# Kernel tuning notes

Measured on AMD Instinct MI355X. Metric: run time of the kernel, lower is better.

The kernel has to match this reference:

```python
import jax, jax.numpy as jnp
import numpy as np

B, D, S = 4, 512, 2048
H, DK = 8, 64  # d_model = H * DK
SCALE = float(np.sqrt(DK))
EPS = 1e-8


def setup_inputs() -> dict:
    key = jax.random.key(0)
    ks = jax.random.split(key, 9)
    std = (2.0 / D) ** 0.5  # kaiming_normal fan_out for 1x1 conv
    inp = {"x": jax.random.normal(ks[0], (B, D, 2, S), dtype=jnp.float32)}
    i = 1
    for n in ("q", "k", "v", "o"):
        inp[f"W{n}_r"] = jax.random.normal(ks[i], (D, D), dtype=jnp.float32) * std
        inp[f"W{n}_i"] = jax.random.normal(ks[i + 1], (D, D), dtype=jnp.float32) * std
        inp[f"b{n}_r"] = jnp.zeros((D,), dtype=jnp.float32)
        inp[f"b{n}_i"] = jnp.zeros((D,), dtype=jnp.float32)
        i += 2
    return inp


def _cconv(x, Wr, Wi, br, bi):
    # complex 1x1 conv: x [B, D, 2, S] -> [B, D, 2, S]
    real, imag = x[:, :, 0, :], x[:, :, 1, :]
    o_r = (jnp.einsum('od,bds->bos', Wr, real)
           - jnp.einsum('od,bds->bos', Wi, imag) + (br - bi)[None, :, None])
    o_i = (jnp.einsum('od,bds->bos', Wr, imag)
           + jnp.einsum('od,bds->bos', Wi, real) + (br + bi)[None, :, None])
    return jnp.stack([o_r, o_i], axis=2)


def reference(x, Wq_r, Wq_i, bq_r, bq_i, Wk_r, Wk_i, bk_r, bk_i,
              Wv_r, Wv_i, bv_r, bv_i, Wo_r, Wo_i, bo_r, bo_i):
    b, c, _, s = x.shape
    Q = _cconv(x, Wq_r, Wq_i, bq_r, bq_i).reshape(b, H, DK, 2, s)
    K = _cconv(x, Wk_r, Wk_i, bk_r, bk_i).reshape(b, H, DK, 2, s)
    V = _cconv(x, Wv_r, Wv_i, bv_r, bv_i).reshape(b, H, DK, 2, s)
    Qm = jnp.sqrt(Q[:, :, :, 0] ** 2 + Q[:, :, :, 1] ** 2 + EPS)  # [b,H,DK,s]
    Km = jnp.sqrt(K[:, :, :, 0] ** 2 + K[:, :, :, 1] ** 2 + EPS)
    scores = jnp.einsum('bhds,bhdt->bhst', Qm, Km) / SCALE  # [b,H,s,s]
    attn = jax.nn.softmax(scores, axis=-1)  # dropout is identity in eval
    Vr = jnp.einsum('bhst,bhdt->bhds', attn, V[:, :, :, 0])  # [b,H,DK,s]
    Vi = jnp.einsum('bhst,bhdt->bhds', attn, V[:, :, :, 1])
    out = jnp.stack([Vr.reshape(b, c, s), Vi.reshape(b, c, s)], axis=2)
    return _cconv(out, Wo_r, Wo_i, bo_r, bo_i)
```

## Files before the change

### kernel.cpp

```cpp
#include <hip/hip_runtime.h>
#include <math.h>
#include <stdint.h>

typedef __attribute__((ext_vector_type(8))) _Float16 f16x8;
typedef __attribute__((ext_vector_type(2))) __fp16 fp16x2;
typedef __attribute__((ext_vector_type(4))) float f32x4;
typedef __attribute__((ext_vector_type(16))) float f32x16;

static __device__ __forceinline__ unsigned short f2h(float f) {
  union { _Float16 h; unsigned short u; } v; v.h = (_Float16)f;
  return v.u;
}
static __device__ __forceinline__ float h2f(unsigned short u) {
  union { unsigned short u; _Float16 h; } v; v.u = u;
  return (float)v.h;
}
static __device__ __forceinline__ unsigned pkrtz(float a, float b) {
  union { fp16x2 h; unsigned u; } v;
  v.h = __builtin_amdgcn_cvt_pkrtz(a, b);
  return v.u;
}

#define GLOAD_LDS16(g, l) __builtin_amdgcn_global_load_lds( \
    (const __attribute__((address_space(1))) void*)(g),     \
    (__attribute__((address_space(3))) void*)(l), 16, 0, 0)

__global__ __launch_bounds__(256) void pack_w(
    const float* __restrict__ Wr, const float* __restrict__ Wi,
    const float* __restrict__ br, const float* __restrict__ bi,
    unsigned short* __restrict__ W2, float* __restrict__ bias2) {
  int idx = blockIdx.x * 256 + threadIdx.x;
  int m = idx >> 10, k = idx & 1023;
  int o = m & 511, d = k & 511;
  float v;
  if (m < 512) v = (k < 512) ? Wr[o * 512 + d] : -Wi[o * 512 + d];
  else         v = (k < 512) ? Wi[o * 512 + d] :  Wr[o * 512 + d];
  W2[idx] = f2h(v);
  if (idx < 1024) {
    int oo = idx & 511;
    bias2[idx] = (idx < 512) ? (br[oo] - bi[oo]) : (br[oo] + bi[oo]);
  }
}

__global__ __launch_bounds__(256) void pack_x(
    const float* __restrict__ x, unsigned short* __restrict__ XT) {
  __shared__ unsigned short tl[64][72];
  const int t = threadIdx.x;
  const int sBase = blockIdx.x * 64, dBase = blockIdx.y * 64;
  const int b = blockIdx.z >> 1, c = blockIdx.z & 1;
  const int r = t >> 2, cb = (t & 3) * 16;
  const float* src = x + (((size_t)(b * 512 + dBase + r) * 2 + c) * 2048 + sBase + cb);
#pragma unroll
  for (int j = 0; j < 16; j += 4) {
    float4 v = *(const float4*)(src + j);
    tl[cb + j + 0][r] = f2h(v.x);
    tl[cb + j + 1][r] = f2h(v.y);
    tl[cb + j + 2][r] = f2h(v.z);
    tl[cb + j + 3][r] = f2h(v.w);
  }
  __syncthreads();
  const int s = t >> 2, dc = (t & 3) * 16;
  unsigned short* dst = XT + ((size_t)(b * 2048 + sBase + s)) * 1024 + c * 512 + dBase + dc;
  *(uint4*)dst = *(const uint4*)&tl[s][dc];
  *(uint4*)(dst + 8) = *(const uint4*)&tl[s][dc + 8];
}

template <int MODE>
__global__ __launch_bounds__(256) void gemm_bt(
    const unsigned short* __restrict__ A, const unsigned short* __restrict__ Bt,
    const float* __restrict__ bias, unsigned short* __restrict__ Cb,
    float* __restrict__ Cf) {
  __shared__ unsigned short As[128 * 32];
  __shared__ unsigned short Bs[128 * 32];
  const int t = threadIdx.x;
  const int wave = t >> 6, lane = t & 63;
  const int wr = wave >> 1, wc = wave & 1;
  const int mBase = blockIdx.y * 128, nBase = blockIdx.x * 128;
  const int z = blockIdx.z;
  A += (size_t)z * 1024 * 1024;
  bias += z * 1024;
  if (MODE == 0) Cb += (size_t)z * 1024 * 8192;
  const int lr = lane & 15, lk = (lane >> 4) * 8;
  f32x4 acc[4][4] = {};
  const int grow = wave * 32 + (lane >> 2);
  const int gcol = (lane & 3) * 8;
  const unsigned short* ga = A + (size_t)(mBase + grow) * 1024 + gcol;
  const unsigned short* gb = Bt + (size_t)(nBase + grow) * 1024 + gcol;
  unsigned short* lA = &As[wave * 1024];
  unsigned short* lB = &Bs[wave * 1024];
  for (int k0 = 0; k0 < 1024; k0 += 32) {
    __syncthreads();
    GLOAD_LDS16(ga + k0, lA);
    GLOAD_LDS16(ga + 16 * 1024 + k0, lA + 512);
    GLOAD_LDS16(gb + k0, lB);
    GLOAD_LDS16(gb + 16 * 1024 + k0, lB + 512);
    __syncthreads();
    f16x8 af[4], bfr[4];
#pragma unroll
    for (int i = 0; i < 4; ++i) {
      af[i]  = *(const f16x8*)&As[(wr * 64 + i * 16 + lr) * 32 + lk];
      bfr[i] = *(const f16x8*)&Bs[(wc * 64 + i * 16 + lr) * 32 + lk];
    }
#pragma unroll
    for (int i = 0; i < 4; ++i)
#pragma unroll
      for (int j = 0; j < 4; ++j)
        acc[i][j] = __builtin_amdgcn_mfma_f32_16x16x32_f16(af[i], bfr[j], acc[i][j], 0, 0, 0);
  }
  const int cr = (lane >> 4) * 4, cc = lane & 15;
#pragma unroll
  for (int i = 0; i < 4; ++i) {
#pragma unroll
    for (int j = 0; j < 4; ++j) {
      const int m0 = mBase + wr * 64 + i * 16 + cr;
      const int n0 = nBase + wc * 64 + j * 16 + cc;
#pragma unroll
      for (int g = 0; g < 4; ++g) {
        float v = acc[i][j][g] + bias[m0 + g];
        if (MODE == 0) {
          const int m = m0 + g;
          if (z == 2) {
            const int ri = m >> 9, mm = m & 511;
            const int h = mm >> 6, dloc = mm & 63;
            const int jj = dloc >> 5, q31 = dloc & 31;
            const int b = n0 >> 11, s = n0 & 2047;
            const int tile = s >> 6, ks = (s >> 4) & 3, hi = (s >> 3) & 1, e = s & 7;
            const size_t flat =
                ((((((size_t)(b * 8 + h) * 32 + tile) * 4 + ks) * 2 + jj) * 2 + ri) * 64 +
                 hi * 32 + q31) * 8 + e;
            Cb[flat] = f2h(v);
          } else {
            Cb[(size_t)m * 8192 + n0] = f2h(v);
          }
        } else {
          const int m = m0 + g;
          const int c = m >> 9, o = m & 511;
          const int b = n0 >> 11, s = n0 & 2047;
          Cf[(size_t)b * 2097152 + (size_t)o * 4096 + c * 2048 + s] = v;
        }
      }
    }
  }
}

__global__ __launch_bounds__(256) void mag_qk(
    const unsigned short* __restrict__ Cq, const unsigned short* __restrict__ Ck,
    unsigned short* __restrict__ Qm, unsigned short* __restrict__ Km) {
  __shared__ unsigned short tl[64][72];
  const int isK = blockIdx.z;
  const unsigned short* C = isK ? Ck : Cq;
  unsigned short* Out = isK ? Km : Qm;
  const int t = threadIdx.x;
  const int sBase = blockIdx.x * 64;
  const int bh = blockIdx.y, b = bh >> 3, h = bh & 7;
  const int d = t >> 2, sc = (t & 3) * 16;
  const unsigned short* pr = C + (size_t)(h * 64 + d) * 8192 + b * 2048 + sBase + sc;
  const unsigned short* pi = pr + (size_t)512 * 8192;
  unsigned short rb[16], ib[16];
  *(uint4*)&rb[0] = *(const uint4*)pr;  *(uint4*)&rb[8] = *(const uint4*)(pr + 8);
  *(uint4*)&ib[0] = *(const uint4*)pi;  *(uint4*)&ib[8] = *(const uint4*)(pi + 8);
#pragma unroll
  for (int j = 0; j < 16; ++j) {
    float fr = h2f(rb[j]), fi = h2f(ib[j]);
    tl[sc + j][d] = f2h(sqrtf(fr * fr + fi * fi + 1e-8f));
  }
  __syncthreads();
  const int s = t >> 2, dc = (t & 3) * 16;
  if (isK) {
    const int kb = s >> 5, q31 = s & 31, db = dc >> 4;
    unsigned short* dstf = Out +
        ((((size_t)bh * 32 + blockIdx.x) * 2 + kb) * 4 + db) * 512 + (size_t)q31 * 8;
    *(uint4*)dstf = *(const uint4*)&tl[s][dc];
    *(uint4*)(dstf + 256) = *(const uint4*)&tl[s][dc + 8];
  } else {
    unsigned short* dst = Out + ((size_t)bh * 2048 + sBase + s) * 64 + dc;
    *(uint4*)dst = *(const uint4*)&tl[s][dc];
    *(uint4*)(dst + 8) = *(const uint4*)&tl[s][dc + 8];
  }
}

__global__ __launch_bounds__(256) void attn(
    const unsigned short* __restrict__ Qm, const unsigned short* __restrict__ Km,
    const unsigned short* __restrict__ Vf, unsigned short* __restrict__ OutT) {
  const int t = threadIdx.x, wave = t >> 6, lane = t & 63;
  const int id = blockIdx.x;
  const int xcd = id & 7, within = id >> 3;
  const int bh = xcd * 4 + (within >> 4);
  const int qtile = within & 15;
  const int b = bh >> 3, h = bh & 7;
  const int q31 = lane & 31, hi = lane >> 5;
  const int qBase = qtile * 128 + wave * 32;
  const float ls = 0.18033688f;

  f16x8 qf[4];
  {
    const unsigned short* qp = Qm + ((size_t)bh * 2048 + qBase + q31) * 64 + hi * 8;
    qf[0] = *(const f16x8*)qp;
    qf[1] = *(const f16x8*)(qp + 16);
    qf[2] = *(const f16x8*)(qp + 32);
    qf[3] = *(const f16x8*)(qp + 48);
  }
  f32x16 Or[2] = {}, Oi[2] = {};
  float m = -1e30f, l = 0.f;

  const unsigned short* kmF = Km + (size_t)bh * 131072 + (size_t)lane * 8;
  const unsigned short* vF  = Vf + (size_t)bh * 262144 + (size_t)lane * 8;

  for (int t0 = 0; t0 < 2048; t0 += 64) {
    const int tile = t0 >> 6;
    f16x8 kf[2][4];
#pragma unroll
    for (int kb = 0; kb < 2; ++kb)
#pragma unroll
      for (int db = 0; db < 4; ++db)
        kf[kb][db] = *(const f16x8*)(kmF + (size_t)(((tile * 2 + kb) * 4 + db)) * 512);
    __builtin_amdgcn_sched_barrier(0);
    f32x16 S[2] = {};
#pragma unroll
    for (int kb = 0; kb < 2; ++kb)
#pragma unroll
      for (int db = 0; db < 4; ++db)
        S[kb] = __builtin_amdgcn_mfma_f32_32x32x16_f16(kf[kb][db], qf[db], S[kb], 0, 0, 0);
    f16x8 vr[4][2], vi[4][2];
#pragma unroll
    for (int ks = 0; ks < 4; ++ks)
#pragma unroll
      for (int j = 0; j < 2; ++j) {
        const size_t u = (size_t)(((tile * 4 + ks) * 2 + j) * 2) * 512;
        vr[ks][j] = *(const f16x8*)(vF + u);
        vi[ks][j] = *(const f16x8*)(vF + u + 512);
      }
    __builtin_amdgcn_sched_barrier(0);
    float m0a = fmaxf(S[0][0], S[0][1]), m0b = fmaxf(S[0][2], S[0][3]);
#pragma unroll
    for (int r = 4; r < 16; r += 4) {
      m0a = fmaxf(m0a, fmaxf(S[0][r], S[0][r + 1]));
      m0b = fmaxf(m0b, fmaxf(S[0][r + 2], S[0][r + 3]));
    }
#pragma unroll
    for (int r = 0; r < 16; r += 4) {
      m0a = fmaxf(m0a, fmaxf(S[1][r], S[1][r + 1]));
      m0b = fmaxf(m0b, fmaxf(S[1][r + 2], S[1][r + 3]));
    }
    float vmax = fmaxf(m0a, m0b);
    vmax = fmaxf(vmax, __shfl_xor(vmax, 32, 64));
    float pmax = vmax * ls;
    if (__any(pmax > m + 8.0f)) {
      float mnew = fmaxf(m, pmax);
      float al = __builtin_amdgcn_exp2f(m - mnew);
      m = mnew;
      l *= al;
#pragma unroll
      for (int r = 0; r < 16; ++r) {
        const int qloc = (r & 3) + 8 * (r >> 2) + 4 * hi;
        float ao = __shfl(al, qloc, 64);
        Or[0][r] *= ao; Or[1][r] *= ao;
        Oi[0][r] *= ao; Oi[1][r] *= ao;
      }
    }
    float p[2][16];
    float ps0 = 0.f, ps1 = 0.f;
#pragma unroll
    for (int kb = 0; kb < 2; ++kb)
#pragma unroll
      for (int r = 0; r < 16; r += 2) {
        float pa_ = __builtin_amdgcn_exp2f(fmaf(S[kb][r], ls, -m));
        float pb_ = __builtin_amdgcn_exp2f(fmaf(S[kb][r + 1], ls, -m));
        p[kb][r] = pa_; p[kb][r + 1] = pb_;
        ps0 += pa_; ps1 += pb_;
      }
    float ps = ps0 + ps1;
    ps += __shfl_xor(ps, 32, 64);
    l += ps;
    f16x8 pa[4];
#pragma unroll
    for (int ks = 0; ks < 4; ++ks) {
      const float* pp = &p[ks >> 1][8 * (ks & 1)];
      unsigned c0 = pkrtz(pp[0], pp[1]);
      unsigned c1 = pkrtz(pp[2], pp[3]);
      unsigned d0 = pkrtz(pp[4], pp[5]);
      unsigned d1 = pkrtz(pp[6], pp[7]);
      asm volatile("v_permlane32_swap_b32 %0, %1" : "+v"(c0), "+v"(d0));
      asm volatile("v_permlane32_swap_b32 %0, %1" : "+v"(c1), "+v"(d1));
      union { unsigned u[4]; f16x8 v; } w;
      w.u[0] = c0; w.u[1] = c1; w.u[2] = d0; w.u[3] = d1;
      pa[ks] = w.v;
    }
#pragma unroll
    for (int ks = 0; ks < 4; ++ks)
#pragma unroll
      for (int j = 0; j < 2; ++j) {
        Or[j] = __builtin_amdgcn_mfma_f32_32x32x16_f16(pa[ks], vr[ks][j], Or[j], 0, 0, 0);
        Oi[j] = __builtin_amdgcn_mfma_f32_32x32x16_f16(pa[ks], vi[ks][j], Oi[j], 0, 0, 0);
      }
  }
  float linv = 1.0f / l;
#pragma unroll
  for (int r = 0; r < 16; ++r) {
    const int qloc = (r & 3) + 8 * (r >> 2) + 4 * hi;
    float iv = __shfl(linv, qloc, 64);
    unsigned short* orow = OutT + ((size_t)b * 2048 + qBase + qloc) * 1024 + h * 64;
    orow[q31]       = f2h(Or[0][r] * iv);
    orow[32 + q31]  = f2h(Or[1][r] * iv);
    orow[512 + q31] = f2h(Oi[0][r] * iv);
    orow[544 + q31] = f2h(Oi[1][r] * iv);
  }
}

extern "C" void kernel_launch(void* const* d_in, const int* in_sizes, int n_in,
                              void* d_out, int out_size, void* d_ws, size_t ws_size,
                              hipStream_t stream) {
  (void)in_sizes; (void)n_in; (void)out_size; (void)ws_size;
  const float* x = (const float*)d_in[0];

  unsigned short* XT = (unsigned short*)d_ws;
  unsigned short* W2 = XT + (size_t)8192 * 1024;
  float* bias2 = (float*)(W2 + (size_t)4 * 1024 * 1024);
  unsigned short* Cqkv = (unsigned short*)(bias2 + 4096);
  unsigned short* Qm = (unsigned short*)d_out;
  unsigned short* Km = Qm + (size_t)4 * 8 * 2048 * 64;
  unsigned short* Vf = Cqkv + (size_t)2 * 1024 * 8192;
  unsigned short* OutT = Cqkv;

  for (int s = 0; s < 4; ++s) {
    pack_w<<<4096, 256, 0, stream>>>(
        (const float*)d_in[1 + 4 * s], (const float*)d_in[2 + 4 * s],
        (const float*)d_in[3 + 4 * s], (const float*)d_in[4 + 4 * s],
        W2 + (size_t)s * 1024 * 1024, bias2 + s * 1024);
  }
  pack_x<<<dim3(32, 8, 8), 256, 0, stream>>>(x, XT);
  gemm_bt<0><<<dim3(64, 8, 3), 256, 0, stream>>>(W2, XT, bias2, Cqkv, nullptr);
  mag_qk<<<dim3(32, 32, 2), 256, 0, stream>>>(Cqkv, Cqkv + (size_t)1024 * 8192, Qm, Km);
  attn<<<512, 256, 0, stream>>>(Qm, Km, Vf, OutT);
  gemm_bt<1><<<dim3(64, 8, 1), 256, 0, stream>>>(
      W2 + (size_t)3 * 1024 * 1024, OutT, bias2 + 3 * 1024, nullptr, (float*)d_out);
}
```

Measured before the change: 209.7 us.

## Split attention over key halves with a combine kernel and XCD-aware GEMM grid

The attention kernel now splits each query tile's key range into two halves, doubling the grid to 1024 blocks for better CU occupancy. Each half writes normalized partial outputs plus its running max and sum, and a new combine kernel merges them with log-sum-exp weights. GEMM launches are flattened to 1D with an XCD-aware block remapping so neighbouring N tiles share an XCD's L2. This adds an extra kernel and extra partial-output traffic, and rounds the partial outputs to fp16 before merging.

```diff
diff --git a/kernel.cpp b/kernel.cpp
--- a/kernel.cpp
+++ b/kernel.cpp
@@ -75,8 +75,11 @@
   const int t = threadIdx.x;
   const int wave = t >> 6, lane = t & 63;
   const int wr = wave >> 1, wc = wave & 1;
-  const int mBase = blockIdx.y * 128, nBase = blockIdx.x * 128;
-  const int z = blockIdx.z;
+  const int bid = blockIdx.x;
+  const int xcd = bid & 7, g = bid >> 3;
+  const int i = g & 63, z = g >> 6;
+  const int nb = xcd * 8 + (i >> 3), mb = i & 7;
+  const int mBase = mb * 128, nBase = nb * 128;
   A += (size_t)z * 1024 * 1024;
   bias += z * 1024;
   if (MODE == 0) Cb += (size_t)z * 1024 * 8192;
@@ -97,28 +100,28 @@
     __syncthreads();
     f16x8 af[4], bfr[4];
 #pragma unroll
-    for (int i = 0; i < 4; ++i) {
-      af[i]  = *(const f16x8*)&As[(wr * 64 + i * 16 + lr) * 32 + lk];
-      bfr[i] = *(const f16x8*)&Bs[(wc * 64 + i * 16 + lr) * 32 + lk];
-    }
-#pragma unroll
-    for (int i = 0; i < 4; ++i)
+    for (int i2 = 0; i2 < 4; ++i2) {
+      af[i2]  = *(const f16x8*)&As[(wr * 64 + i2 * 16 + lr) * 32 + lk];
+      bfr[i2] = *(const f16x8*)&Bs[(wc * 64 + i2 * 16 + lr) * 32 + lk];
+    }
+#pragma unroll
+    for (int i2 = 0; i2 < 4; ++i2)
 #pragma unroll
       for (int j = 0; j < 4; ++j)
-        acc[i][j] = __builtin_amdgcn_mfma_f32_16x16x32_f16(af[i], bfr[j], acc[i][j], 0, 0, 0);
+        acc[i2][j] = __builtin_amdgcn_mfma_f32_16x16x32_f16(af[i2], bfr[j], acc[i2][j], 0, 0, 0);
   }
   const int cr = (lane >> 4) * 4, cc = lane & 15;
 #pragma unroll
-  for (int i = 0; i < 4; ++i) {
+  for (int i2 = 0; i2 < 4; ++i2) {
 #pragma unroll
     for (int j = 0; j < 4; ++j) {
-      const int m0 = mBase + wr * 64 + i * 16 + cr;
+      const int m0 = mBase + wr * 64 + i2 * 16 + cr;
       const int n0 = nBase + wc * 64 + j * 16 + cc;
 #pragma unroll
-      for (int g = 0; g < 4; ++g) {
-        float v = acc[i][j][g] + bias[m0 + g];
+      for (int g2 = 0; g2 < 4; ++g2) {
+        float v = acc[i2][j][g2] + bias[m0 + g2];
         if (MODE == 0) {
-          const int m = m0 + g;
+          const int m = m0 + g2;
           if (z == 2) {
             const int ri = m >> 9, mm = m & 511;
             const int h = mm >> 6, dloc = mm & 63;
@@ -133,7 +136,7 @@
             Cb[(size_t)m * 8192 + n0] = f2h(v);
           }
         } else {
-          const int m = m0 + g;
+          const int m = m0 + g2;
           const int c = m >> 9, o = m & 511;
           const int b = n0 >> 11, s = n0 & 2047;
           Cf[(size_t)b * 2097152 + (size_t)o * 4096 + c * 2048 + s] = v;
@@ -181,12 +184,14 @@
 
 __global__ __launch_bounds__(256) void attn(
     const unsigned short* __restrict__ Qm, const unsigned short* __restrict__ Km,
-    const unsigned short* __restrict__ Vf, unsigned short* __restrict__ OutT) {
+    const unsigned short* __restrict__ Vf, unsigned short* __restrict__ Op0,
+    unsigned short* __restrict__ Op1, float2* __restrict__ ml) {
   const int t = threadIdx.x, wave = t >> 6, lane = t & 63;
   const int id = blockIdx.x;
   const int xcd = id & 7, within = id >> 3;
-  const int bh = xcd * 4 + (within >> 4);
-  const int qtile = within & 15;
+  const int bh = xcd * 4 + (within >> 5);
+  const int rem = within & 31;
+  const int qtile = rem >> 1, half = rem & 1;
   const int b = bh >> 3, h = bh & 7;
   const int q31 = lane & 31, hi = lane >> 5;
   const int qBase = qtile * 128 + wave * 32;
@@ -203,17 +208,17 @@
   f32x16 Or[2] = {}, Oi[2] = {};
   float m = -1e30f, l = 0.f;
 
-  const unsigned short* kmF = Km + (size_t)bh * 131072 + (size_t)lane * 8;
-  const unsigned short* vF  = Vf + (size_t)bh * 262144 + (size_t)lane * 8;
-
-  for (int t0 = 0; t0 < 2048; t0 += 64) {
-    const int tile = t0 >> 6;
+  const int tile0 = half * 16;
+  const unsigned short* kptr = Km + (size_t)bh * 131072 + (size_t)tile0 * 4096 + (size_t)lane * 8;
+  const unsigned short* vptr = Vf + (size_t)bh * 262144 + (size_t)tile0 * 8192 + (size_t)lane * 8;
+
+  for (int it = 0; it < 16; ++it) {
     f16x8 kf[2][4];
 #pragma unroll
     for (int kb = 0; kb < 2; ++kb)
 #pragma unroll
       for (int db = 0; db < 4; ++db)
-        kf[kb][db] = *(const f16x8*)(kmF + (size_t)(((tile * 2 + kb) * 4 + db)) * 512);
+        kf[kb][db] = *(const f16x8*)(kptr + (size_t)(kb * 4 + db) * 512);
     __builtin_amdgcn_sched_barrier(0);
     f32x16 S[2] = {};
 #pragma unroll
@@ -226,11 +231,12 @@
     for (int ks = 0; ks < 4; ++ks)
 #pragma unroll
       for (int j = 0; j < 2; ++j) {
-        const size_t u = (size_t)(((tile * 4 + ks) * 2 + j) * 2) * 512;
-        vr[ks][j] = *(const f16x8*)(vF + u);
-        vi[ks][j] = *(const f16x8*)(vF + u + 512);
+        const size_t u = (size_t)((ks * 2 + j) * 2) * 512;
+        vr[ks][j] = *(const f16x8*)(vptr + u);
+        vi[ks][j] = *(const f16x8*)(vptr + u + 512);
       }
     __builtin_amdgcn_sched_barrier(0);
+    kptr += 4096; vptr += 8192;
     float m0a = fmaxf(S[0][0], S[0][1]), m0b = fmaxf(S[0][2], S[0][3]);
 #pragma unroll
     for (int r = 4; r < 16; r += 4) {
@@ -294,16 +300,53 @@
         Oi[j] = __builtin_amdgcn_mfma_f32_32x32x16_f16(pa[ks], vi[ks][j], Oi[j], 0, 0, 0);
       }
   }
+  unsigned short* Op = half ? Op1 : Op0;
   float linv = 1.0f / l;
 #pragma unroll
   for (int r = 0; r < 16; ++r) {
     const int qloc = (r & 3) + 8 * (r >> 2) + 4 * hi;
     float iv = __shfl(linv, qloc, 64);
-    unsigned short* orow = OutT + ((size_t)b * 2048 + qBase + qloc) * 1024 + h * 64;
+    unsigned short* orow = Op + ((size_t)b * 2048 + qBase + qloc) * 1024 + h * 64;
     orow[q31]       = f2h(Or[0][r] * iv);
     orow[32 + q31]  = f2h(Or[1][r] * iv);
     orow[512 + q31] = f2h(Oi[0][r] * iv);
     orow[544 + q31] = f2h(Oi[1][r] * iv);
+  }
+  if (hi == 0) {
+    float2 v; v.x = m; v.y = l;
+    ml[(size_t)half * 65536 + (size_t)bh * 2048 + qBase + q31] = v;
+  }
+}
+
+__global__ __launch_bounds__(256) void combine(
+    const unsigned short* __restrict__ O0, const unsigned short* __restrict__ O1,
+    const float2* __restrict__ ml, unsigned short* __restrict__ OutT) {
+  const int tid = blockIdx.x * 256 + threadIdx.x;
+  const int d4 = tid & 3, h = (tid >> 2) & 7, c = (tid >> 5) & 1;
+  const int q = (tid >> 6) & 2047, b = tid >> 17;
+  const size_t bhq = (size_t)(b * 8 + h) * 2048 + q;
+  float2 ml0 = ml[bhq];
+  float2 ml1 = ml[65536 + bhq];
+  float M = fmaxf(ml0.x, ml1.x);
+  float w0 = ml0.y * exp2f(ml0.x - M);
+  float w1 = ml1.y * exp2f(ml1.x - M);
+  float inv = 1.0f / (w0 + w1);
+  float s0 = w0 * inv, s1 = w1 * inv;
+  const size_t off = ((size_t)b * 2048 + q) * 1024 + c * 512 + h * 64 + d4 * 16;
+  const unsigned short* p0 = O0 + off;
+  const unsigned short* p1 = O1 + off;
+  unsigned short* po = OutT + off;
+#pragma unroll
+  for (int g = 0; g < 2; ++g) {
+    uint4 a = *(const uint4*)(p0 + g * 8);
+    uint4 bb = *(const uint4*)(p1 + g * 8);
+    const unsigned short* ap = (const unsigned short*)&a;
+    const unsigned short* bp = (const unsigned short*)&bb;
+    unsigned short r[8];
+#pragma unroll
+    for (int e = 0; e < 8; ++e)
+      r[e] = f2h(s0 * h2f(ap[e]) + s1 * h2f(bp[e]));
+    *(uint4*)(po + g * 8) = *(const uint4*)r;
   }
 }
 
@@ -319,6 +362,9 @@
   unsigned short* Cqkv = (unsigned short*)(bias2 + 4096);
   unsigned short* Qm = (unsigned short*)d_out;
   unsigned short* Km = Qm + (size_t)4 * 8 * 2048 * 64;
+  unsigned short* Op0 = XT;
+  unsigned short* Op1 = Km + (size_t)4 * 8 * 2048 * 64;
+  float2* ml = (float2*)(Cqkv + (size_t)1024 * 8192);
   unsigned short* Vf = Cqkv + (size_t)2 * 1024 * 8192;
   unsigned short* OutT = Cqkv;
 
@@ -329,9 +375,10 @@
         W2 + (size_t)s * 1024 * 1024, bias2 + s * 1024);
   }
   pack_x<<<dim3(32, 8, 8), 256, 0, stream>>>(x, XT);
-  gemm_bt<0><<<dim3(64, 8, 3), 256, 0, stream>>>(W2, XT, bias2, Cqkv, nullptr);
+  gemm_bt<0><<<1536, 256, 0, stream>>>(W2, XT, bias2, Cqkv, nullptr);
   mag_qk<<<dim3(32, 32, 2), 256, 0, stream>>>(Cqkv, Cqkv + (size_t)1024 * 8192, Qm, Km);
-  attn<<<512, 256, 0, stream>>>(Qm, Km, Vf, OutT);
-  gemm_bt<1><<<dim3(64, 8, 1), 256, 0, stream>>>(
+  attn<<<1024, 256, 0, stream>>>(Qm, Km, Vf, Op0, Op1, ml);
+  combine<<<2048, 256, 0, stream>>>(Op0, Op1, ml, OutT);
+  gemm_bt<1><<<512, 256, 0, stream>>>(
       W2 + (size_t)3 * 1024 * 1024, OutT, bias2 + 3 * 1024, nullptr, (float*)d_out);
 }
```

Result: slower. 235.2 us (+12.1%).
